# Optimization experiments

Hardware: AMD Instinct MI355X
Metric: run time of the kernel (lower is better)

Reference implementation:

```python
import jax, jax.numpy as jnp
import numpy as np

GAMMA = 10.0    # norm_output gamma for the softmax mask
EPS_BN = 1e-5   # BatchNorm eps
EPS_L2 = 1e-8   # l2norm eps (lavse adds eps to the norm)


def l2norm(x, axis):
    n = jnp.sqrt(jnp.sum(x * x, axis=axis, keepdims=True)) + EPS_L2
    return x / n


def setup_inputs() -> dict:
    key = jax.random.key(0)
    ks = jax.random.split(key, 8)
    Bi, R, D, Bc, T, H = 64, 36, 1024, 32, 64, 128  # H = latent_size // k
    return {
        "img_embed": jax.random.normal(ks[0], (Bi, R, D), jnp.float32),
        "cap_embed": jax.random.normal(ks[1], (Bc, T, D), jnp.float32),
        "Wg1": jax.random.normal(ks[2], (D, H), jnp.float32) * 0.02,
        "bg1": jnp.zeros((H,), jnp.float32),
        "Wg2": jax.random.normal(ks[3], (H, D), jnp.float32) * 0.02,
        "bg2": jnp.zeros((D,), jnp.float32),
        "Wb1": jax.random.normal(ks[4], (D, H), jnp.float32) * 0.02,
        "bb1": jnp.zeros((H,), jnp.float32),
        "Wb2": jax.random.normal(ks[5], (H, D), jnp.float32) * 0.02,
        "bb2": jnp.zeros((D,), jnp.float32),
        "lens": jax.random.randint(ks[6], (Bc,), 4, T - 4, jnp.int32),
    }


def reference(img_embed, cap_embed, Wg1, bg1, Wg2, bg2, Wb1, bb1, Wb2, bb2, lens):
    # cap_embed: (Bc, T, D); ragged mean-pool over the first lens[i] words
    Bc, T, D = cap_embed.shape
    mask = (jnp.arange(T)[None, :] < lens[:, None]).astype(cap_embed.dtype)  # (Bc, T)
    cap_repr = jnp.einsum('btd,bt->bd', cap_embed, mask) / lens[:, None].astype(cap_embed.dtype)

    # img_embed: (Bi, R, D) -> (Bi, D, R); BatchNorm1d (no affine) with batch stats
    x = jnp.transpose(img_embed, (0, 2, 1))
    mean = jnp.mean(x, axis=(0, 2), keepdims=True)          # per-channel over (Bi, R)
    var = jnp.mean((x - mean) ** 2, axis=(0, 2), keepdims=True)
    bn = (x - mean) * jax.lax.rsqrt(var + EPS_BN)           # (Bi, D, R)

    # conditional gamma/beta predicted from each caption vector (1024->128->1024)
    gammas = jax.nn.relu(cap_repr @ Wg1 + bg1) @ Wg2 + bg2  # (Bc, D)
    betas = jax.nn.relu(cap_repr @ Wb1 + bb1) @ Wb2 + bb2   # (Bc, D)

    # vectorized over captions: the torch code loops per caption
    out = bn[None] * gammas[:, None, :, None] + betas[:, None, :, None]  # (Bc, Bi, D, R)
    m = jax.nn.softmax(out * GAMMA, axis=-1)                # softmax mask over regions
    out = m * out

    img_vec = l2norm(jnp.mean(out, axis=-1), -1)            # (Bc, Bi, D)
    cap_vec = l2norm(cap_repr, -1)                          # (Bc, D)
    sims = jnp.einsum('cbd,cd->bc', img_vec, cap_vec)       # (Bi, Bc)
    return sims
```

## Files before the change

kernel.cpp:

```cpp
#include <hip/hip_runtime.h>
#include <math.h>

#define DD 1024
#define HD 128
#define BI 64
#define RR 36
#define BC 32
#define TT 64

#define EPS_BN 1e-5f
#define EPS_L2 1e-8f
#define GAMMA_SM 10.0f
#define LOG2E 1.44269504088896f
#define CEXP (GAMMA_SM * LOG2E)

#define NBN 64
#define ROWS_BN 36

__global__ __launch_bounds__(256) void k1(const float* __restrict__ cap,
                                          const int* __restrict__ lens,
                                          const float* __restrict__ img,
                                          const float* __restrict__ Wg1,
                                          const float* __restrict__ Wb1,
                                          float* __restrict__ bnpart,
                                          float* __restrict__ repr,
                                          float* __restrict__ sqpart,
                                          float* __restrict__ hp) {
    int bid = blockIdx.x, tid = threadIdx.x;
    if (bid < 512) {
        int e = bid;
        int c = e >> 4, kc = e & 15;
        int len = lens[c];
        __shared__ float4 red[16][17];
        __shared__ float rs[64];
        __shared__ float sqs[16];
        int j = tid & 15, tg = tid >> 4;
        const float4* cp = reinterpret_cast<const float4*>(cap + (size_t)c * TT * DD + kc * 64) + j;
        float4 s = {0.f, 0.f, 0.f, 0.f};
#pragma unroll
        for (int i = 0; i < 4; i++) {
            int t = tg + i * 16;
            if (t < len) {
                float4 x = cp[(size_t)t * 256];
                s.x += x.x; s.y += x.y; s.z += x.z; s.w += x.w;
            }
        }
        red[tg][j] = s;
        __syncthreads();
#pragma unroll
        for (int off = 8; off > 0; off >>= 1) {
            if (tg < off) {
                float4 o = red[tg + off][j];
                red[tg][j].x += o.x; red[tg][j].y += o.y;
                red[tg][j].z += o.z; red[tg][j].w += o.w;
            }
            __syncthreads();
        }
        if (tid < 16) {
            float inv = 1.0f / (float)len;
            float4 v = red[0][tid];
            v.x *= inv; v.y *= inv; v.z *= inv; v.w *= inv;
            rs[tid * 4 + 0] = v.x;
            rs[tid * 4 + 1] = v.y;
            rs[tid * 4 + 2] = v.z;
            rs[tid * 4 + 3] = v.w;
            reinterpret_cast<float4*>(repr)[c * 256 + kc * 16 + tid] = v;
            sqs[tid] = fmaf(v.x, v.x, fmaf(v.y, v.y, fmaf(v.z, v.z, v.w * v.w)));
        }
        __syncthreads();
        if (tid == 0) {
            float s2 = 0.f;
#pragma unroll
            for (int k = 0; k < 16; k++) s2 += sqs[k];
            sqpart[c * 16 + kc] = s2;
        }
        int gb = tid >> 7, h = tid & (HD - 1);
        const float* Wp = (gb ? Wb1 : Wg1) + (size_t)(kc * 64) * HD + h;
        float a0 = 0.f, a1 = 0.f, a2 = 0.f, a3 = 0.f;
#pragma unroll
        for (int d = 0; d < 64; d += 4) {
            a0 = fmaf(rs[d + 0], Wp[(size_t)(d + 0) * HD], a0);
            a1 = fmaf(rs[d + 1], Wp[(size_t)(d + 1) * HD], a1);
            a2 = fmaf(rs[d + 2], Wp[(size_t)(d + 2) * HD], a2);
            a3 = fmaf(rs[d + 3], Wp[(size_t)(d + 3) * HD], a3);
        }
        hp[(size_t)e * 256 + tid] = (a0 + a1) + (a2 + a3);
    } else {
        int g = bid - 512;
        const float4* p = reinterpret_cast<const float4*>(img) + (size_t)g * ROWS_BN * 256 + tid;
        float4 s = {0.f, 0.f, 0.f, 0.f}, q = {0.f, 0.f, 0.f, 0.f};
#pragma unroll
        for (int i = 0; i < ROWS_BN; i++) {
            float4 x = p[(size_t)i * 256];
            s.x += x.x; s.y += x.y; s.z += x.z; s.w += x.w;
            q.x = fmaf(x.x, x.x, q.x); q.y = fmaf(x.y, x.y, q.y);
            q.z = fmaf(x.z, x.z, q.z); q.w = fmaf(x.w, x.w, q.w);
        }
        float4* bp = reinterpret_cast<float4*>(bnpart);
        bp[(g * 2 + 0) * 256 + tid] = s;
        bp[(g * 2 + 1) * 256 + tid] = q;
    }
}

__global__ __launch_bounds__(256) void k2(const float* __restrict__ bnpart,
                                          const float* __restrict__ hp,
                                          const float* __restrict__ bg1,
                                          const float* __restrict__ bb1,
                                          const float* __restrict__ Wg2,
                                          const float* __restrict__ bg2,
                                          const float* __restrict__ Wb2,
                                          const float* __restrict__ bb2,
                                          float* __restrict__ Ap,
                                          float* __restrict__ Bp) {
    int c = blockIdx.x >> 3, dg = blockIdx.x & 7;
    int tid = threadIdx.x;
    int gb = tid >> 7, h = tid & (HD - 1);
    __shared__ float hid[256], ex2[256], sred[256], qred[256];

    {
        int d = dg * HD + h;
        float s = 0.f, q = 0.f;
        const float* bp = bnpart + (size_t)(gb * 32) * 2 * DD + d;
#pragma unroll
        for (int g = 0; g < 32; g++) {
            s += bp[(size_t)(g * 2 + 0) * DD];
            q += bp[(size_t)(g * 2 + 1) * DD];
        }
        sred[tid] = s;
        qred[tid] = q;
    }
    {
        const float* hpp = hp + (size_t)c * 16 * 256 + tid;
        float s = 0.f;
#pragma unroll
        for (int k = 0; k < 16; k++) s += hpp[k * 256];
        hid[tid] = fmaxf(s + (gb ? bb1[h] : bg1[h]), 0.f);
    }
    __syncthreads();
    int d = dg * HD + h;
    const float* Wp = (gb ? Wb2 : Wg2) + d;
    const float* hs = hid + gb * HD;
    float a0 = 0.f, a1 = 0.f, a2 = 0.f, a3 = 0.f;
    float a4 = 0.f, a5 = 0.f, a6 = 0.f, a7 = 0.f;
#pragma unroll
    for (int hh = 0; hh < HD; hh += 8) {
        a0 = fmaf(hs[hh + 0], Wp[(size_t)(hh + 0) * DD], a0);
        a1 = fmaf(hs[hh + 1], Wp[(size_t)(hh + 1) * DD], a1);
        a2 = fmaf(hs[hh + 2], Wp[(size_t)(hh + 2) * DD], a2);
        a3 = fmaf(hs[hh + 3], Wp[(size_t)(hh + 3) * DD], a3);
        a4 = fmaf(hs[hh + 4], Wp[(size_t)(hh + 4) * DD], a4);
        a5 = fmaf(hs[hh + 5], Wp[(size_t)(hh + 5) * DD], a5);
        a6 = fmaf(hs[hh + 6], Wp[(size_t)(hh + 6) * DD], a6);
        a7 = fmaf(hs[hh + 7], Wp[(size_t)(hh + 7) * DD], a7);
    }
    ex2[tid] = ((a0 + a1) + (a2 + a3)) + ((a4 + a5) + (a6 + a7))
               + (gb ? bb2[d] : bg2[d]);
    __syncthreads();
    if (tid < HD) {
        const float invN = 1.0f / (float)(BI * RR);
        float s = sred[tid] + sred[tid + HD];
        float q = qred[tid] + qred[tid + HD];
        float m = s * invN;
        float rstd = rsqrtf(fmaf(-m, m, q * invN) + EPS_BN);
        float a = ex2[tid] * rstd;
        float bv = fmaf(-m, a, ex2[tid + HD]);
        Ap[c * DD + d] = a * CEXP;
        Bp[c * DD + d] = bv * CEXP;
    }
}

__global__ __launch_bounds__(512, 4) void k3(const float* __restrict__ img,
                                             const float* __restrict__ Ap,
                                             const float* __restrict__ Bp,
                                             const float* __restrict__ repr,
                                             const float* __restrict__ sqpart,
                                             float* __restrict__ sims) {
    int b = blockIdx.x, cg = blockIdx.y;
    int tid = threadIdx.x;
    int lane = tid & 63, wid = tid >> 6;
    __shared__ float invn_l[4];
    if (tid < 64) {
        float v = sqpart[(cg * 4 + (tid >> 4)) * 16 + (tid & 15)];
#pragma unroll
        for (int off = 8; off > 0; off >>= 1) v += __shfl_down(v, off);
        if ((tid & 15) == 0) invn_l[tid >> 4] = 1.0f / (sqrtf(v) + EPS_L2);
    }
    const float2* ip = reinterpret_cast<const float2*>(img + (size_t)b * RR * DD) + tid;
    float2 x[RR];
#pragma unroll
    for (int r = 0; r < RR; r++) x[r] = ip[(size_t)r * 512];
    __shared__ float sq_l[8][4], dt_l[8][4];
    const float invRC = 1.0f / ((float)RR * CEXP);
    for (int ci = 0; ci < 4; ci++) {
        int c = cg * 4 + ci;
        float2 ap = reinterpret_cast<const float2*>(Ap)[c * 512 + tid];
        float2 bp = reinterpret_cast<const float2*>(Bp)[c * 512 + tid];
        float2 cn = reinterpret_cast<const float2*>(repr)[c * 512 + tid];
        float sex = 0.f, sey = 0.f, sox = 0.f, soy = 0.f;
#pragma unroll
        for (int r = 0; r < RR; r++) {
            float ox = fmaf(ap.x, x[r].x, bp.x);
            float oy = fmaf(ap.y, x[r].y, bp.y);
            float ex_ = exp2f(ox);
            float ey = exp2f(oy);
            sex += ex_; sey += ey;
            sox = fmaf(ex_, ox, sox);
            soy = fmaf(ey, oy, soy);
        }
        float vx = sox / sex * invRC;
        float vy = soy / sey * invRC;
        float sq = fmaf(vx, vx, vy * vy);
        float dt = fmaf(vx, cn.x, vy * cn.y);
#pragma unroll
        for (int off = 32; off > 0; off >>= 1) {
            sq += __shfl_down(sq, off);
            dt += __shfl_down(dt, off);
        }
        if (lane == 0) { sq_l[wid][ci] = sq; dt_l[wid][ci] = dt; }
    }
    __syncthreads();
    if (tid < 4) {
        float sq = 0.f, dt = 0.f;
#pragma unroll
        for (int w = 0; w < 8; w++) { sq += sq_l[w][tid]; dt += dt_l[w][tid]; }
        sims[b * BC + cg * 4 + tid] = dt * invn_l[tid] / (sqrtf(sq) + EPS_L2);
    }
}

extern "C" void kernel_launch(void* const* d_in, const int* in_sizes, int n_in,
                              void* d_out, int out_size, void* d_ws, size_t ws_size,
                              hipStream_t stream) {
    const float* img = (const float*)d_in[0];
    const float* cap = (const float*)d_in[1];
    const float* Wg1 = (const float*)d_in[2];
    const float* bg1 = (const float*)d_in[3];
    const float* Wg2 = (const float*)d_in[4];
    const float* bg2 = (const float*)d_in[5];
    const float* Wb1 = (const float*)d_in[6];
    const float* bb1 = (const float*)d_in[7];
    const float* Wb2 = (const float*)d_in[8];
    const float* bb2 = (const float*)d_in[9];
    const int* lens = (const int*)d_in[10];
    float* out = (float*)d_out;

    float* ws = (float*)d_ws;
    float* repr   = ws;
    float* sqpart = ws + 32768;
    float* hp     = ws + 33792;
    float* bnpart = ws + 164864;
    float* Ap     = ws + 295936;
    float* Bp     = ws + 328704;

    k1<<<576, 256, 0, stream>>>(cap, lens, img, Wg1, Wb1,
                                bnpart, repr, sqpart, hp);
    k2<<<256, 256, 0, stream>>>(bnpart, hp, bg1, bb1, Wg2, bg2, Wb2, bb2,
                                Ap, Bp);
    k3<<<dim3(BI, 8), 512, 0, stream>>>(img, Ap, Bp, repr, sqpart, out);
}
```

Measured before the change: 40.30 us.

## Fuse k1 and k2 into one kernel with an atomic-counter grid barrier

Merges the caption-pooling/BN-partial kernel and the gamma/beta MLP kernel into a single launch. Blocks increment a global counter when their first phase is done, and the first 256 blocks spin until all 576 have arrived before running the second phase. This removes one kernel launch and its inter-kernel gap, but adds a memset launch and a spin-wait that relies on all 576 blocks being co-resident or otherwise scheduled so the barrier completes.

```diff
diff --git a/kernel.cpp b/kernel.cpp
--- a/kernel.cpp
+++ b/kernel.cpp
@@ -14,26 +14,36 @@
 #define LOG2E 1.44269504088896f
 #define CEXP (GAMMA_SM * LOG2E)
 
-#define NBN 64
 #define ROWS_BN 36
-
-__global__ __launch_bounds__(256) void k1(const float* __restrict__ cap,
-                                          const int* __restrict__ lens,
-                                          const float* __restrict__ img,
-                                          const float* __restrict__ Wg1,
-                                          const float* __restrict__ Wb1,
-                                          float* __restrict__ bnpart,
-                                          float* __restrict__ repr,
-                                          float* __restrict__ sqpart,
-                                          float* __restrict__ hp) {
+#define NBLK 576
+
+__global__ __launch_bounds__(256) void k12(const float* __restrict__ cap,
+                                           const int* __restrict__ lens,
+                                           const float* __restrict__ img,
+                                           const float* __restrict__ Wg1,
+                                           const float* __restrict__ Wb1,
+                                           const float* __restrict__ bg1,
+                                           const float* __restrict__ bb1,
+                                           const float* __restrict__ Wg2,
+                                           const float* __restrict__ bg2,
+                                           const float* __restrict__ Wb2,
+                                           const float* __restrict__ bb2,
+                                           float* __restrict__ bnpart,
+                                           float* __restrict__ repr,
+                                           float* __restrict__ sqpart,
+                                           float* __restrict__ hp,
+                                           float* __restrict__ Ap,
+                                           float* __restrict__ Bp,
+                                           int* __restrict__ cnt) {
     int bid = blockIdx.x, tid = threadIdx.x;
+    __shared__ float4 red[16][17];
+    __shared__ float rs[64];
+    __shared__ float sqs[16];
+    __shared__ float hid[256], ex2[256], sred[256], qred[256];
+
     if (bid < 512) {
-        int e = bid;
-        int c = e >> 4, kc = e & 15;
+        int c = bid >> 4, kc = bid & 15;
         int len = lens[c];
-        __shared__ float4 red[16][17];
-        __shared__ float rs[64];
-        __shared__ float sqs[16];
         int j = tid & 15, tg = tid >> 4;
         const float4* cp = reinterpret_cast<const float4*>(cap + (size_t)c * TT * DD + kc * 64) + j;
         float4 s = {0.f, 0.f, 0.f, 0.f};
@@ -84,7 +94,7 @@
             a2 = fmaf(rs[d + 2], Wp[(size_t)(d + 2) * HD], a2);
             a3 = fmaf(rs[d + 3], Wp[(size_t)(d + 3) * HD], a3);
         }
-        hp[(size_t)e * 256 + tid] = (a0 + a1) + (a2 + a3);
+        hp[(size_t)bid * 256 + tid] = (a0 + a1) + (a2 + a3);
     } else {
         int g = bid - 512;
         const float4* p = reinterpret_cast<const float4*>(img) + (size_t)g * ROWS_BN * 256 + tid;
@@ -100,23 +110,20 @@
         bp[(g * 2 + 0) * 256 + tid] = s;
         bp[(g * 2 + 1) * 256 + tid] = q;
     }
-}
-
-__global__ __launch_bounds__(256) void k2(const float* __restrict__ bnpart,
-                                          const float* __restrict__ hp,
-                                          const float* __restrict__ bg1,
-                                          const float* __restrict__ bb1,
-                                          const float* __restrict__ Wg2,
-                                          const float* __restrict__ bg2,
-                                          const float* __restrict__ Wb2,
-                                          const float* __restrict__ bb2,
-                                          float* __restrict__ Ap,
-                                          float* __restrict__ Bp) {
-    int c = blockIdx.x >> 3, dg = blockIdx.x & 7;
-    int tid = threadIdx.x;
+
+    __syncthreads();
+    __threadfence();
+    if (tid == 0) atomicAdd(cnt, 1);
+    if (bid >= 256) return;
+    if (tid == 0) {
+        while (__hip_atomic_load(cnt, __ATOMIC_ACQUIRE, __HIP_MEMORY_SCOPE_AGENT) < NBLK)
+            __builtin_amdgcn_s_sleep(8);
+    }
+    __syncthreads();
+    __threadfence();
+
+    int c = bid >> 3, dg = bid & 7;
     int gb = tid >> 7, h = tid & (HD - 1);
-    __shared__ float hid[256], ex2[256], sred[256], qred[256];
-
     {
         int d = dg * HD + h;
         float s = 0.f, q = 0.f;
@@ -250,10 +257,11 @@
     float* bnpart = ws + 164864;
     float* Ap     = ws + 295936;
     float* Bp     = ws + 328704;
-
-    k1<<<576, 256, 0, stream>>>(cap, lens, img, Wg1, Wb1,
-                                bnpart, repr, sqpart, hp);
-    k2<<<256, 256, 0, stream>>>(bnpart, hp, bg1, bb1, Wg2, bg2, Wb2, bb2,
-                                Ap, Bp);
+    int*   cnt    = (int*)(ws + 361472);
+
+    hipMemsetAsync((void*)cnt, 0, sizeof(int), stream);
+    k12<<<NBLK, 256, 0, stream>>>(cap, lens, img, Wg1, Wb1,
+                                  bg1, bb1, Wg2, bg2, Wb2, bb2,
+                                  bnpart, repr, sqpart, hp, Ap, Bp, cnt);
     k3<<<dim3(BI, 8), 512, 0, stream>>>(img, Ap, Bp, repr, sqpart, out);
 }
```

Measured after the change: 134.1 us. 233% more time.
